# Performance work log

Hardware: AMD Instinct MI355X
Metric: run time of the kernel (lower is better)

Reference implementation:

```python
import jax, jax.numpy as jnp
import numpy as np

EPS = 0.2          # noise scale (init eps)
N_LAYERS = 3
LAYER_CL = 1
USER_NUM = 100000
ITEM_NUM = 50000
NNZ = 1200000
EMB = 64


def setup_inputs() -> dict:
    key = jax.random.key(0)
    k1, k2, k3, k4, k5, k6 = jax.random.split(key, 6)
    N = USER_NUM + ITEM_NUM
    user_emb = jax.random.normal(k1, (USER_NUM, EMB), dtype=jnp.float32)
    item_emb = jax.random.normal(k2, (ITEM_NUM, EMB), dtype=jnp.float32)
    adj_rows = jax.random.randint(k3, (NNZ,), 0, N, dtype=jnp.int32)
    adj_cols = jax.random.randint(k4, (NNZ,), 0, N, dtype=jnp.int32)
    adj_vals = jax.random.uniform(k5, (NNZ,), dtype=jnp.float32)
    noise = jax.random.uniform(k6, (N_LAYERS, N, EMB), dtype=jnp.float32)  # torch.rand_like per layer
    return {"user_emb": user_emb, "item_emb": item_emb, "adj_rows": adj_rows,
            "adj_cols": adj_cols, "adj_vals": adj_vals, "noise": noise}


def _l2_normalize(x):
    # F.normalize(x, dim=-1): x / max(||x||_2, 1e-12)
    n = jnp.sqrt(jnp.sum(x * x, axis=-1, keepdims=True))
    return x / jnp.maximum(n, 1e-12)


def reference(user_emb, item_emb, adj_rows, adj_cols, adj_vals, noise):
    N = user_emb.shape[0] + item_emb.shape[0]
    ego = jnp.concatenate([user_emb, item_emb], axis=0)  # [N, D]
    acc = jnp.zeros_like(ego)
    cl = ego
    for k in range(N_LAYERS):
        # SpMM: ego <- A @ ego (COO via gather + segment_sum)
        gathered = ego[adj_cols] * adj_vals[:, None]          # [nnz, D]
        ego = jax.ops.segment_sum(gathered, adj_rows, num_segments=N)
        # perturbed=True path: signed, l2-normalized uniform noise
        ego = ego + jnp.sign(ego) * _l2_normalize(noise[k]) * EPS
        acc = acc + ego
        if k == LAYER_CL - 1:
            cl = ego
    final = acc / N_LAYERS  # mean over layers (stack+mean fused)
    u = final[:user_emb.shape[0]]
    i = final[user_emb.shape[0]:]
    u_cl = cl[:user_emb.shape[0]]
    i_cl = cl[user_emb.shape[0]:]
    return (u, i, u_cl, i_cl)
```

## Files before the change

kernel.cpp:

```cpp
#include <hip/hip_runtime.h>
#include <hip/hip_bf16.h>

#define EPSV 0.2f
#define USER_NUM 100000
#define ITEM_NUM 50000
#define NTOT 150000
#define NNZ_CNT 1200000
#define EMB 64
#define SCAN_BS 256
#define NBLK ((NTOT + SCAN_BS - 1) / SCAN_BS)


__global__ void hist_kernel(const int* __restrict__ rows,
                            int* __restrict__ hist,
                            int* __restrict__ ticket) {
    int e = blockIdx.x * blockDim.x + threadIdx.x;
    if (e < NNZ_CNT) ticket[e] = atomicAdd(&hist[rows[e]], 1);
}

__global__ void scan_local_kernel(const int* __restrict__ hist,
                                  int* __restrict__ rowstart,
                                  int* __restrict__ blocksum) {
    __shared__ int s[SCAN_BS];
    int t = threadIdx.x;
    int i = blockIdx.x * SCAN_BS + t;
    int v = (i < NTOT) ? hist[i] : 0;
    s[t] = v;
    __syncthreads();
    for (int off = 1; off < SCAN_BS; off <<= 1) {
        int x = (t >= off) ? s[t - off] : 0;
        __syncthreads();
        s[t] += x;
        __syncthreads();
    }
    if (i < NTOT) rowstart[i] = s[t] - v;
    if (t == SCAN_BS - 1) blocksum[blockIdx.x] = s[t];
}

__global__ void scan_block_kernel(int* __restrict__ blocksum) {
    __shared__ int s[1024];
    int t = threadIdx.x;
    int v = (t < NBLK) ? blocksum[t] : 0;
    s[t] = v;
    __syncthreads();
    for (int off = 1; off < 1024; off <<= 1) {
        int x = (t >= off) ? s[t - off] : 0;
        __syncthreads();
        s[t] += x;
        __syncthreads();
    }
    if (t < NBLK) blocksum[t] = s[t] - v;
}

__global__ void scan_add_kernel(int* __restrict__ rowstart,
                                const int* __restrict__ blockoff) {
    int i = blockIdx.x * blockDim.x + threadIdx.x;
    if (i < NTOT) rowstart[i] += blockoff[i / SCAN_BS];
    if (i == 0) rowstart[NTOT] = NNZ_CNT;
}

__global__ void build_kernel(const int* __restrict__ rows,
                             const int* __restrict__ cols,
                             const float* __restrict__ vals,
                             const int* __restrict__ rowstart,
                             const int* __restrict__ ticket,
                             int2* __restrict__ csr) {
    int e = blockIdx.x * blockDim.x + threadIdx.x;
    if (e >= NNZ_CNT) return;
    int r = rows[e];
    int slot = rowstart[r] + ticket[e];
    csr[slot] = make_int2(cols[e], __float_as_int(vals[e]));
}

template <bool CONCAT>
__global__ void spmm_perturb_kernel(const float* __restrict__ src,
                                    const float* __restrict__ user_emb,
                                    const float* __restrict__ item_emb,
                                    const int* __restrict__ rowstart,
                                    const int2* __restrict__ csr,
                                    const float* __restrict__ noise_k,
                                    float* __restrict__ ego_out,
                                    float* __restrict__ final_out,
                                    int store_ego, int first_layer) {
    int row = blockIdx.x * 4 + (threadIdx.x >> 6);
    row = __builtin_amdgcn_readfirstlane(row);
    if (row >= NTOT) return;
    int lane = threadIdx.x & 63;
    size_t idx = (size_t)row * EMB + lane;
    float nv = noise_k[idx];
    int beg = rowstart[row];
    int end = rowstart[row + 1];
    float acc = 0.f;
    for (int j = beg; j < end; j += 8) {
        int   cb[8];
        float vb[8];
        #pragma unroll
        for (int u = 0; u < 8; ++u) {
            int jj = j + u;
            int2 ee = csr[(jj < end) ? jj : (end - 1)];
            cb[u] = ee.x;
            vb[u] = (jj < end) ? __int_as_float(ee.y) : 0.f;
        }
        float xb[8];
        #pragma unroll
        for (int u = 0; u < 8; ++u) {
            int c = cb[u];
            const float* base;
            if (CONCAT)
                base = (c < USER_NUM) ? (user_emb + (size_t)c * EMB)
                                      : (item_emb + (size_t)(c - USER_NUM) * EMB);
            else
                base = src + (size_t)c * EMB;
            xb[u] = base[lane];
        }
        #pragma unroll
        for (int u = 0; u < 8; ++u) acc = fmaf(vb[u], xb[u], acc);
    }
    float s = nv * nv;
    #pragma unroll
    for (int off = 32; off > 0; off >>= 1) s += __shfl_xor(s, off, 64);
    float nn = nv / fmaxf(sqrtf(s), 1e-12f);
    float sg = (acc > 0.f) ? 1.f : ((acc < 0.f) ? -1.f : 0.f);
    float y = acc + sg * nn * EPSV;
    if (store_ego) ego_out[idx] = y;
    const float third = 1.f / 3.f;
    if (first_layer) final_out[idx] = y * third;
    else             final_out[idx] += y * third;
}

extern "C" void kernel_launch(void* const* d_in, const int* in_sizes, int n_in,
                              void* d_out, int out_size, void* d_ws, size_t ws_size,
                              hipStream_t stream) {
    const float* user_emb = (const float*)d_in[0];
    const float* item_emb = (const float*)d_in[1];
    const int*   adj_rows = (const int*)d_in[2];
    const int*   adj_cols = (const int*)d_in[3];
    const float* adj_vals = (const float*)d_in[4];
    const float* noise    = (const float*)d_in[5];

    float* out_final = (float*)d_out;
    float* out_cl    = (float*)d_out + (size_t)NTOT * EMB;

    char* p = (char*)d_ws;
    float* wsA      = (float*)p;  p += (size_t)NTOT * EMB * sizeof(float);
    int*   rowstart = (int*)p;    p += (size_t)(NTOT + 16) * sizeof(int);
    int2*  csr      = (int2*)p;   p += (size_t)NNZ_CNT * sizeof(int2);
    int*   hist     = (int*)p;    p += (size_t)NTOT * sizeof(int);
    int*   ticket   = (int*)p;    p += (size_t)NNZ_CNT * sizeof(int);
    int*   blocksum = (int*)p;    p += 1024 * sizeof(int);

    hipMemsetAsync(hist, 0, (size_t)NTOT * sizeof(int), stream);

    hist_kernel<<<(NNZ_CNT + 255) / 256, 256, 0, stream>>>(adj_rows, hist, ticket);
    scan_local_kernel<<<NBLK, SCAN_BS, 0, stream>>>(hist, rowstart, blocksum);
    scan_block_kernel<<<1, 1024, 0, stream>>>(blocksum);
    scan_add_kernel<<<(NTOT + 255) / 256, 256, 0, stream>>>(rowstart, blocksum);
    build_kernel<<<(NNZ_CNT + 255) / 256, 256, 0, stream>>>(
        adj_rows, adj_cols, adj_vals, rowstart, ticket, csr);

    const int spmm_blocks = (NTOT + 3) / 4;
    const size_t NE = (size_t)NTOT * EMB;

    spmm_perturb_kernel<true><<<spmm_blocks, 256, 0, stream>>>(
        nullptr, user_emb, item_emb, rowstart, csr, noise + 0 * NE,
        out_cl, out_final, 1, 1);
    spmm_perturb_kernel<false><<<spmm_blocks, 256, 0, stream>>>(
        out_cl, nullptr, nullptr, rowstart, csr, noise + 1 * NE,
        wsA, out_final, 1, 0);
    spmm_perturb_kernel<false><<<spmm_blocks, 256, 0, stream>>>(
        wsA, nullptr, nullptr, rowstart, csr, noise + 2 * NE,
        wsA, out_final, 0, 0);
}
```

Measured before the change: 493.2 us.

## Map four rows per wavefront with float4 gathers and single-pass atomic row allocation

The SpMM kernel now assigns four rows to each 64-lane wavefront, with 16 lanes per row each loading a float4. Gathers and noise/output traffic become 16-byte vector accesses, and each wave overlaps four rows' CSR traversal. The three-kernel prefix scan is replaced by one kernel that does a wave-level scan and takes an atomic base offset per block, producing (start,end) row ranges. The CSR rows are therefore no longer laid out in row order, and divergence across the four rows in a wave can leave lanes idle.

```diff
diff --git a/kernel.cpp b/kernel.cpp
--- a/kernel.cpp
+++ b/kernel.cpp
@@ -7,8 +7,6 @@
 #define NTOT 150000
 #define NNZ_CNT 1200000
 #define EMB 64
-#define SCAN_BS 256
-#define NBLK ((NTOT + SCAN_BS - 1) / SCAN_BS)
 
 
 __global__ void hist_kernel(const int* __restrict__ rows,
@@ -18,57 +16,50 @@
     if (e < NNZ_CNT) ticket[e] = atomicAdd(&hist[rows[e]], 1);
 }
 
-__global__ void scan_local_kernel(const int* __restrict__ hist,
-                                  int* __restrict__ rowstart,
-                                  int* __restrict__ blocksum) {
-    __shared__ int s[SCAN_BS];
+__global__ __launch_bounds__(1024) void alloc_kernel(const int* __restrict__ hist,
+                                                     int2* __restrict__ rowrange,
+                                                     int* __restrict__ cnt) {
+    __shared__ int wsum[16];
+    __shared__ int sbase;
     int t = threadIdx.x;
-    int i = blockIdx.x * SCAN_BS + t;
-    int v = (i < NTOT) ? hist[i] : 0;
-    s[t] = v;
+    int i = blockIdx.x * 1024 + t;
+    int deg = (i < NTOT) ? hist[i] : 0;
+    int lane = t & 63;
+    int wid = t >> 6;
+    int inc = deg;
+    #pragma unroll
+    for (int off = 1; off < 64; off <<= 1) {
+        int x = __shfl_up(inc, off, 64);
+        if (lane >= off) inc += x;
+    }
+    if (lane == 63) wsum[wid] = inc;
     __syncthreads();
-    for (int off = 1; off < SCAN_BS; off <<= 1) {
-        int x = (t >= off) ? s[t - off] : 0;
-        __syncthreads();
-        s[t] += x;
-        __syncthreads();
+    if (t < 16) {
+        int v = wsum[t];
+        #pragma unroll
+        for (int off = 1; off < 16; off <<= 1) {
+            int x = __shfl_up(v, off, 64);
+            if (t >= off) v += x;
+        }
+        wsum[t] = v;
+        if (t == 15) sbase = atomicAdd(cnt, v);
     }
-    if (i < NTOT) rowstart[i] = s[t] - v;
-    if (t == SCAN_BS - 1) blocksum[blockIdx.x] = s[t];
-}
-
-__global__ void scan_block_kernel(int* __restrict__ blocksum) {
-    __shared__ int s[1024];
-    int t = threadIdx.x;
-    int v = (t < NBLK) ? blocksum[t] : 0;
-    s[t] = v;
     __syncthreads();
-    for (int off = 1; off < 1024; off <<= 1) {
-        int x = (t >= off) ? s[t - off] : 0;
-        __syncthreads();
-        s[t] += x;
-        __syncthreads();
-    }
-    if (t < NBLK) blocksum[t] = s[t] - v;
-}
-
-__global__ void scan_add_kernel(int* __restrict__ rowstart,
-                                const int* __restrict__ blockoff) {
-    int i = blockIdx.x * blockDim.x + threadIdx.x;
-    if (i < NTOT) rowstart[i] += blockoff[i / SCAN_BS];
-    if (i == 0) rowstart[NTOT] = NNZ_CNT;
+    int waveoff = (wid > 0) ? wsum[wid - 1] : 0;
+    int excl = sbase + waveoff + inc - deg;
+    if (i < NTOT) rowrange[i] = make_int2(excl, excl + deg);
 }
 
 __global__ void build_kernel(const int* __restrict__ rows,
                              const int* __restrict__ cols,
                              const float* __restrict__ vals,
-                             const int* __restrict__ rowstart,
+                             const int2* __restrict__ rowrange,
                              const int* __restrict__ ticket,
                              int2* __restrict__ csr) {
     int e = blockIdx.x * blockDim.x + threadIdx.x;
     if (e >= NNZ_CNT) return;
     int r = rows[e];
-    int slot = rowstart[r] + ticket[e];
+    int slot = rowrange[r].x + ticket[e];
     csr[slot] = make_int2(cols[e], __float_as_int(vals[e]));
 }
 
@@ -76,32 +67,33 @@
 __global__ void spmm_perturb_kernel(const float* __restrict__ src,
                                     const float* __restrict__ user_emb,
                                     const float* __restrict__ item_emb,
-                                    const int* __restrict__ rowstart,
+                                    const int2* __restrict__ rowrange,
                                     const int2* __restrict__ csr,
                                     const float* __restrict__ noise_k,
                                     float* __restrict__ ego_out,
                                     float* __restrict__ final_out,
                                     int store_ego, int first_layer) {
-    int row = blockIdx.x * 4 + (threadIdx.x >> 6);
-    row = __builtin_amdgcn_readfirstlane(row);
+    int wid = threadIdx.x >> 6;
+    int lane = threadIdx.x & 63;
+    int rsub = lane >> 4;
+    int q = lane & 15;
+    int row = blockIdx.x * 16 + wid * 4 + rsub;
     if (row >= NTOT) return;
-    int lane = threadIdx.x & 63;
-    size_t idx = (size_t)row * EMB + lane;
-    float nv = noise_k[idx];
-    int beg = rowstart[row];
-    int end = rowstart[row + 1];
-    float acc = 0.f;
+    int2 rr = rowrange[row];
+    int beg = rr.x, end = rr.y;
+    size_t rowoff = (size_t)row * EMB;
+    float4 nv = ((const float4*)(noise_k + rowoff))[q];
+    float4 acc = make_float4(0.f, 0.f, 0.f, 0.f);
     for (int j = beg; j < end; j += 8) {
-        int   cb[8];
+        int cb[8];
         float vb[8];
         #pragma unroll
         for (int u = 0; u < 8; ++u) {
             int jj = j + u;
-            int2 ee = csr[(jj < end) ? jj : (end - 1)];
+            int2 ee = csr[(jj < end) ? jj : beg];
             cb[u] = ee.x;
             vb[u] = (jj < end) ? __int_as_float(ee.y) : 0.f;
         }
-        float xb[8];
         #pragma unroll
         for (int u = 0; u < 8; ++u) {
             int c = cb[u];
@@ -111,21 +103,33 @@
                                       : (item_emb + (size_t)(c - USER_NUM) * EMB);
             else
                 base = src + (size_t)c * EMB;
-            xb[u] = base[lane];
+            float4 x = ((const float4*)base)[q];
+            acc.x = fmaf(vb[u], x.x, acc.x);
+            acc.y = fmaf(vb[u], x.y, acc.y);
+            acc.z = fmaf(vb[u], x.z, acc.z);
+            acc.w = fmaf(vb[u], x.w, acc.w);
         }
-        #pragma unroll
-        for (int u = 0; u < 8; ++u) acc = fmaf(vb[u], xb[u], acc);
     }
-    float s = nv * nv;
+    float s = nv.x * nv.x + nv.y * nv.y + nv.z * nv.z + nv.w * nv.w;
     #pragma unroll
-    for (int off = 32; off > 0; off >>= 1) s += __shfl_xor(s, off, 64);
-    float nn = nv / fmaxf(sqrtf(s), 1e-12f);
-    float sg = (acc > 0.f) ? 1.f : ((acc < 0.f) ? -1.f : 0.f);
-    float y = acc + sg * nn * EPSV;
-    if (store_ego) ego_out[idx] = y;
+    for (int off = 8; off > 0; off >>= 1) s += __shfl_xor(s, off, 64);
+    float scale = EPSV / fmaxf(sqrtf(s), 1e-12f);
+    auto pert = [&](float a, float n) {
+        float sg = (a > 0.f) ? 1.f : ((a < 0.f) ? -1.f : 0.f);
+        return fmaf(sg * scale, n, a);
+    };
+    float4 y = make_float4(pert(acc.x, nv.x), pert(acc.y, nv.y),
+                           pert(acc.z, nv.z), pert(acc.w, nv.w));
+    if (store_ego) ((float4*)(ego_out + rowoff))[q] = y;
     const float third = 1.f / 3.f;
-    if (first_layer) final_out[idx] = y * third;
-    else             final_out[idx] += y * third;
+    float4* fin4 = (float4*)(final_out + rowoff);
+    if (first_layer) {
+        fin4[q] = make_float4(y.x * third, y.y * third, y.z * third, y.w * third);
+    } else {
+        float4 o = fin4[q];
+        fin4[q] = make_float4(o.x + y.x * third, o.y + y.y * third,
+                              o.z + y.z * third, o.w + y.w * third);
+    }
 }
 
 extern "C" void kernel_launch(void* const* d_in, const int* in_sizes, int n_in,
@@ -143,31 +147,29 @@
 
     char* p = (char*)d_ws;
     float* wsA      = (float*)p;  p += (size_t)NTOT * EMB * sizeof(float);
-    int*   rowstart = (int*)p;    p += (size_t)(NTOT + 16) * sizeof(int);
+    int2*  rowrange = (int2*)p;   p += (size_t)NTOT * sizeof(int2);
     int2*  csr      = (int2*)p;   p += (size_t)NNZ_CNT * sizeof(int2);
+    int*   ticket   = (int*)p;    p += (size_t)NNZ_CNT * sizeof(int);
     int*   hist     = (int*)p;    p += (size_t)NTOT * sizeof(int);
-    int*   ticket   = (int*)p;    p += (size_t)NNZ_CNT * sizeof(int);
-    int*   blocksum = (int*)p;    p += 1024 * sizeof(int);
+    int*   cnt      = (int*)p;    p += 16 * sizeof(int);
 
-    hipMemsetAsync(hist, 0, (size_t)NTOT * sizeof(int), stream);
+    hipMemsetAsync(hist, 0, ((size_t)NTOT + 16) * sizeof(int), stream);
 
     hist_kernel<<<(NNZ_CNT + 255) / 256, 256, 0, stream>>>(adj_rows, hist, ticket);
-    scan_local_kernel<<<NBLK, SCAN_BS, 0, stream>>>(hist, rowstart, blocksum);
-    scan_block_kernel<<<1, 1024, 0, stream>>>(blocksum);
-    scan_add_kernel<<<(NTOT + 255) / 256, 256, 0, stream>>>(rowstart, blocksum);
+    alloc_kernel<<<(NTOT + 1023) / 1024, 1024, 0, stream>>>(hist, rowrange, cnt);
     build_kernel<<<(NNZ_CNT + 255) / 256, 256, 0, stream>>>(
-        adj_rows, adj_cols, adj_vals, rowstart, ticket, csr);
+        adj_rows, adj_cols, adj_vals, rowrange, ticket, csr);
 
-    const int spmm_blocks = (NTOT + 3) / 4;
+    const int spmm_blocks = (NTOT + 15) / 16;
     const size_t NE = (size_t)NTOT * EMB;
 
     spmm_perturb_kernel<true><<<spmm_blocks, 256, 0, stream>>>(
-        nullptr, user_emb, item_emb, rowstart, csr, noise + 0 * NE,
+        nullptr, user_emb, item_emb, rowrange, csr, noise + 0 * NE,
         out_cl, out_final, 1, 1);
     spmm_perturb_kernel<false><<<spmm_blocks, 256, 0, stream>>>(
-        out_cl, nullptr, nullptr, rowstart, csr, noise + 1 * NE,
+        out_cl, nullptr, nullptr, rowrange, csr, noise + 1 * NE,
         wsA, out_final, 1, 0);
     spmm_perturb_kernel<false><<<spmm_blocks, 256, 0, stream>>>(
-        wsA, nullptr, nullptr, rowstart, csr, noise + 2 * NE,
+        wsA, nullptr, nullptr, rowrange, csr, noise + 2 * NE,
         wsA, out_final, 0, 0);
 }
```

New measurement: 454.7 us. 1.08x faster.
